# Kernel tuning notes

Measured on AMD Instinct MI355X. Metric: run time of the kernel, lower is better.

Reference implementation:

```python
import jax, jax.numpy as jnp
import numpy as np

B, T, D, H = 2, 2048, 768, 12
HD = D // H  # head_dim = 64


def setup_inputs() -> dict:
    key = jax.random.key(0)
    ks = jax.random.split(key, 5)
    s = 0.02
    return {
        "x": jax.random.normal(ks[0], (B, T, D), dtype=jnp.float32),
        "w_qkv": jax.random.normal(ks[1], (D, 3 * D), dtype=jnp.float32) * s,
        "b_qkv": jax.random.normal(ks[2], (3 * D,), dtype=jnp.float32) * s,
        "w_out": jax.random.normal(ks[3], (D, D), dtype=jnp.float32) * s,
        "b_out": jax.random.normal(ks[4], (D,), dtype=jnp.float32) * s,
    }


def reference(x, w_qkv, b_qkv, w_out, b_out):
    Bx, Tx, C = x.shape
    qkv = x @ w_qkv + b_qkv                       # [B,T,3C]
    q, k, v = jnp.split(qkv, 3, axis=-1)
    # [B,H,T,hd]
    q = q.reshape(Bx, Tx, H, HD).transpose(0, 2, 1, 3)
    k = k.reshape(Bx, Tx, H, HD).transpose(0, 2, 1, 3)
    v = v.reshape(Bx, Tx, H, HD).transpose(0, 2, 1, 3)
    scale = 1.0 / jnp.sqrt(jnp.float32(HD))
    attn = jnp.einsum('bhqd,bhkd->bhqk', q, k) * scale  # [B,H,T,T]
    causal = jnp.tril(jnp.ones((Tx, Tx), dtype=bool))
    attn = jnp.where(causal, attn, -jnp.inf)
    attn = jax.nn.softmax(attn, axis=-1)
    y = jnp.einsum('bhqk,bhkd->bhqd', attn, v)          # [B,H,T,hd]
    y = y.transpose(0, 2, 1, 3).reshape(Bx, Tx, C)
    return y @ w_out + b_out
```

## Files before the change

### kernel.cpp

```cpp
#include <hip/hip_runtime.h>
#include <math.h>

typedef __attribute__((ext_vector_type(8))) __bf16 bf16x8;
typedef __attribute__((ext_vector_type(4))) __bf16 bf16x4;
typedef __attribute__((ext_vector_type(4))) float f32x4;

#define GLOAD_LDS16(gsrc, ldst) \
  __builtin_amdgcn_global_load_lds((__attribute__((address_space(1))) const void*)(gsrc), \
                                   (__attribute__((address_space(3))) void*)(ldst), 16, 0, 0)

__device__ __forceinline__ float fexp2(float x) {
#if __has_builtin(__builtin_amdgcn_exp2f)
  return __builtin_amdgcn_exp2f(x);
#else
  return exp2f(x);
#endif
}

__global__ void cvt_bf16_kernel(const float* __restrict__ in, __bf16* __restrict__ out, int n4) {
  int i = blockIdx.x * 256 + threadIdx.x;
  if (i < n4) {
    float4 f = ((const float4*)in)[i];
    bf16x4 o;
    o[0] = (__bf16)f.x; o[1] = (__bf16)f.y; o[2] = (__bf16)f.z; o[3] = (__bf16)f.w;
    ((bf16x4*)out)[i] = o;
  }
}

__global__ __launch_bounds__(256)
void cvtT_bf16_kernel(const float* __restrict__ in, __bf16* __restrict__ out, int R, int C) {
  __shared__ float t[32][33];
  int c0 = blockIdx.x * 32, r0 = blockIdx.y * 32;
  int tc = threadIdx.x & 31, tr = threadIdx.x >> 5;
#pragma unroll
  for (int i = 0; i < 4; ++i)
    t[tr + 8 * i][tc] = in[(size_t)(r0 + tr + 8 * i) * C + c0 + tc];
  __syncthreads();
#pragma unroll
  for (int i = 0; i < 4; ++i)
    out[(size_t)(c0 + tr + 8 * i) * R + r0 + tc] = (__bf16)t[tc][tr + 8 * i];
}

template<int EPI, int BM, int BN, int WAVES, int WGM, int WGN, int BUFS>
__global__ __launch_bounds__(WAVES * 64, 3)
void gemm_tn_kernel(const __bf16* __restrict__ A, const __bf16* __restrict__ Bm,
                    const float* __restrict__ bias, float* __restrict__ outF,
                    __bf16* __restrict__ qo, __bf16* __restrict__ ko, __bf16* __restrict__ vo,
                    int M, int N, int K, int NBX, int NNX, int PPX) {
  constexpr int NTA = BM / 16, NTB = BN / 16;
  constexpr int NA = 2 * NTA;
  constexpr int NSEG = 2 * NTA + 2 * NTB;
  constexpr int LPTH = (NSEG + WAVES - 1) / WAVES;
  constexpr int LPTR = NSEG % WAVES;
  constexpr int LLO = (LPTR == 0) ? LPTH : LPTH - 1;
  constexpr int AM = NTA / WGM;
  constexpr int BNF = NTB / WGN;
  const int lane = threadIdx.x & 63;
  const int wave = threadIdx.x >> 6;
  const int r16 = lane & 15, g = lane >> 4;
  const int id = blockIdx.x;
  const int xcd = id & 7, slot = id >> 3;
  const int nxn = NBX / NNX;
  const int mg = xcd / nxn, ng = xcd % nxn;
  const int lp = slot / NNX, ln = slot - (slot / NNX) * NNX;
  const int mBase = (mg * PPX + lp) * BM, nBase = (ng * NNX + ln) * BN;
  __shared__ __align__(16) __bf16 lds[BUFS][NSEG * 512];

  f32x4 acc[AM][BNF];
#pragma unroll
  for (int i = 0; i < AM; ++i)
#pragma unroll
    for (int j = 0; j < BNF; ++j) acc[i][j] = (f32x4){0.f, 0.f, 0.f, 0.f};

  const int mw = (wave / WGN) * AM;
  const int nw = (wave % WGN) * BNF;

  auto stage = [&](int ke, int b) {
#pragma unroll
    for (int i = 0; i < LPTH; ++i) {
      int s = wave + i * WAVES;
      if (LPTR == 0 || s < NSEG) {
        int isB = (s >= NA);
        int sb = isB ? s - NA : s;
        int nt = isB ? NTB : NTA;
        int ks = sb / nt, t8 = sb - ks * nt;
        int row = (isB ? nBase : mBase) + t8 * 16 + r16;
        const __bf16* src = (isB ? Bm : A) + (size_t)row * K + ke + ks * 32 + g * 8;
        GLOAD_LDS16(src, &lds[b][s * 512]);
      }
    }
  };

  auto mfma_step = [&](const __bf16* L) {
#pragma unroll
    for (int ks = 0; ks < 2; ++ks) {
      bf16x8 af[AM], bfr[BNF];
#pragma unroll
      for (int i = 0; i < AM; ++i)
        af[i] = *(const bf16x8*)&L[((ks * NTA + mw + i) * 64 + lane) * 8];
#pragma unroll
      for (int j = 0; j < BNF; ++j)
        bfr[j] = *(const bf16x8*)&L[((NA + ks * NTB + nw + j) * 64 + lane) * 8];
      __builtin_amdgcn_s_setprio(1);
#pragma unroll
      for (int i = 0; i < AM; ++i)
#pragma unroll
        for (int j = 0; j < BNF; ++j)
          acc[i][j] = __builtin_amdgcn_mfma_f32_16x16x32_bf16(af[i], bfr[j], acc[i][j], 0, 0, 0);
      __builtin_amdgcn_s_setprio(0);
    }
  };

  const int nt = K >> 6;
  if constexpr (BUFS == 2) {
    stage(0, 0);
    int cur = 0;
    for (int t = 0; t < nt; ++t) {
      __syncthreads();
      if (t + 1 < nt) stage((t + 1) << 6, cur ^ 1);
      mfma_step(lds[cur]);
      cur ^= 1;
    }
  } else {
    stage(0, 0);
    stage(64, 1);
    int cur = 0;
    for (int t = 0; t < nt; ++t) {
      if (t + 1 < nt) {
        if (LPTR != 0 && wave < LPTR) asm volatile("s_waitcnt vmcnt(%0)" :: "i"(LPTH) : "memory");
        else                          asm volatile("s_waitcnt vmcnt(%0)" :: "i"(LLO) : "memory");
      } else {
        asm volatile("s_waitcnt vmcnt(0)" ::: "memory");
      }
      __builtin_amdgcn_sched_barrier(0);
      __builtin_amdgcn_s_barrier();
      __builtin_amdgcn_sched_barrier(0);
      int nxt = cur + 2; if (nxt >= 3) nxt -= 3;
      if (t + 2 < nt) stage((t + 2) << 6, nxt);
      mfma_step(lds[cur]);
      if (++cur == 3) cur = 0;
    }
  }

#pragma unroll
  for (int i = 0; i < AM; ++i) {
#pragma unroll
    for (int j = 0; j < BNF; ++j) {
      int c = nBase + (nw + j) * 16 + r16;
      float bb = bias[c];
#pragma unroll
      for (int e = 0; e < 4; ++e) {
        int r = mBase + (mw + i) * 16 + g * 4 + e;
        float val = acc[i][j][e] + bb;
        if (EPI == 0) {
          int which = c / 768;
          int cc = c - which * 768;
          int hh = cc >> 6, dd = cc & 63;
          int bI = r >> 11, tt = r & 2047;
          if (which == 0) {
            qo[(((size_t)(bI * 12 + hh)) * 2048 + tt) * 64 + dd] = (__bf16)(val * 0.180336880f);
          } else if (which == 1) {
            ko[(((size_t)(bI * 12 + hh)) * 2048 + tt) * 64 + dd] = (__bf16)val;
          } else {
            vo[(((size_t)(bI * 12 + hh)) * 64 + dd) * 2048 + tt] = (__bf16)val;
          }
        } else {
          outF[(size_t)r * N + c] = val;
        }
      }
    }
  }
}

__global__ __launch_bounds__(256, 3)
void attn_kernel(const __bf16* __restrict__ qg, const __bf16* __restrict__ kg,
                 const __bf16* __restrict__ vtg, __bf16* __restrict__ yatt) {
  const int id = blockIdx.x;
  const int chunk = id & 7, within = id >> 3;
  const int bh = chunk * 3 + (within >> 4);
  const int u = within & 15;
  const int lane = threadIdx.x & 63, wave = threadIdx.x >> 6;
  const int r16 = lane & 15, g = lane >> 4;
  const int bI = bh / 12, h = bh - bI * 12;
  const size_t headoff = (size_t)bh * 2048 * 64;
  const __bf16* Q = qg + headoff;
  const __bf16* Kh = kg + headoff;
  const __bf16* VT = vtg + headoff;

  __shared__ __align__(16) __bf16 Kbuf[2][4096];
  __shared__ __align__(16) __bf16 Vbuf[2][4096];
  __shared__ __align__(16) __bf16 Plds[4][16][72];

  const int myTile = (wave == 0) ? (63 - 2 * u) : (wave == 1) ? (62 - 2 * u)
                   : (wave == 2) ? (2 * u)      : (2 * u + 1);
  const int myKt = (myTile >> 1) + 1;
  const int Kmax = 32 - u;

  const int row0 = myTile * 32 + r16;
  const int row1 = myTile * 32 + 16 + r16;

  bf16x8 qf[2][2];
#pragma unroll
  for (int ks = 0; ks < 2; ++ks) {
    qf[0][ks] = *(const bf16x8*)&Q[(size_t)row0 * 64 + ks * 32 + g * 8];
    qf[1][ks] = *(const bf16x8*)&Q[(size_t)row1 * 64 + ks * 32 + g * 8];
  }

  int srow[2], scl[2];
#pragma unroll
  for (int i = 0; i < 2; ++i) {
    int c = (i * 4 + wave) * 64 + lane;
    srow[i] = c >> 3;
    scl[i] = (c & 7) ^ (srow[i] & 7);
  }
  auto stage = [&](int kt, int b) {
#pragma unroll
    for (int i = 0; i < 2; ++i) {
      GLOAD_LDS16(&Kh[(size_t)(kt * 64 + srow[i]) * 64 + scl[i] * 8], &Kbuf[b][(i * 4 + wave) * 512]);
      GLOAD_LDS16(&VT[(size_t)srow[i] * 2048 + kt * 64 + scl[i] * 8], &Vbuf[b][(i * 4 + wave) * 512]);
    }
  };

  f32x4 o0[4], o1[4];
#pragma unroll
  for (int j = 0; j < 4; ++j) { o0[j] = (f32x4){0.f,0.f,0.f,0.f}; o1[j] = (f32x4){0.f,0.f,0.f,0.f}; }
  float l0 = 0.f, l1 = 0.f;

  stage(0, 0);
  for (int kt = 0; kt < Kmax; ++kt) {
    const int cur = kt & 1;
    __syncthreads();
    if (kt + 1 < Kmax) stage(kt + 1, cur ^ 1);
    if (kt < myKt) {
      f32x4 st0[4], st1[4];
#pragma unroll
      for (int j = 0; j < 4; ++j) { st0[j] = (f32x4){0.f,0.f,0.f,0.f}; st1[j] = (f32x4){0.f,0.f,0.f,0.f}; }
      __builtin_amdgcn_s_setprio(1);
#pragma unroll
      for (int ks = 0; ks < 2; ++ks)
#pragma unroll
        for (int j = 0; j < 4; ++j) {
          int row = j * 16 + r16;
          int cp = (ks * 4 + g) ^ (row & 7);
          bf16x8 kf = *(const bf16x8*)&Kbuf[cur][(row * 8 + cp) * 8];
          st0[j] = __builtin_amdgcn_mfma_f32_16x16x32_bf16(kf, qf[0][ks], st0[j], 0, 0, 0);
          st1[j] = __builtin_amdgcn_mfma_f32_16x16x32_bf16(kf, qf[1][ks], st1[j], 0, 0, 0);
        }
      __builtin_amdgcn_s_setprio(0);
      bf16x8 vf[2][4];
#pragma unroll
      for (int ks = 0; ks < 2; ++ks)
#pragma unroll
        for (int dj = 0; dj < 4; ++dj) {
          int row = dj * 16 + r16;
          int cp = (ks * 4 + g) ^ (row & 7);
          vf[ks][dj] = *(const bf16x8*)&Vbuf[cur][(row * 8 + cp) * 8];
        }
      const bool lastT = (kt == myKt - 1);
      if (lastT) {
#pragma unroll
        for (int j = 0; j < 4; ++j)
#pragma unroll
          for (int e = 0; e < 4; ++e) {
            int k = kt * 64 + j * 16 + 4 * g + e;
            if (k > row0) st0[j][e] = -INFINITY;
            if (k > row1) st1[j][e] = -INFINITY;
          }
      }
      float ls0 = 0.f, ls1 = 0.f;
#pragma unroll
      for (int j = 0; j < 4; ++j)
#pragma unroll
        for (int e = 0; e < 4; ++e) {
          float p0 = fexp2(st0[j][e]);
          float p1 = fexp2(st1[j][e]);
          st0[j][e] = p0; ls0 += p0;
          st1[j][e] = p1; ls1 += p1;
        }
      ls0 += __shfl_xor(ls0, 16, 64); ls0 += __shfl_xor(ls0, 32, 64); l0 += ls0;
      ls1 += __shfl_xor(ls1, 16, 64); ls1 += __shfl_xor(ls1, 32, 64); l1 += ls1;
#pragma unroll
      for (int j = 0; j < 4; ++j) {
        bf16x4 pk;
#pragma unroll
        for (int e = 0; e < 4; ++e) pk[e] = (__bf16)st0[j][e];
        *(bf16x4*)&Plds[wave][r16][j * 16 + 4 * g] = pk;
      }
      __builtin_amdgcn_s_setprio(1);
#pragma unroll
      for (int ks = 0; ks < 2; ++ks) {
        bf16x8 pf = *(const bf16x8*)&Plds[wave][r16][ks * 32 + g * 8];
#pragma unroll
        for (int dj = 0; dj < 4; ++dj)
          o0[dj] = __builtin_amdgcn_mfma_f32_16x16x32_bf16(vf[ks][dj], pf, o0[dj], 0, 0, 0);
      }
      __builtin_amdgcn_s_setprio(0);
#pragma unroll
      for (int j = 0; j < 4; ++j) {
        bf16x4 pk;
#pragma unroll
        for (int e = 0; e < 4; ++e) pk[e] = (__bf16)st1[j][e];
        *(bf16x4*)&Plds[wave][r16][j * 16 + 4 * g] = pk;
      }
      __builtin_amdgcn_s_setprio(1);
#pragma unroll
      for (int ks = 0; ks < 2; ++ks) {
        bf16x8 pf = *(const bf16x8*)&Plds[wave][r16][ks * 32 + g * 8];
#pragma unroll
        for (int dj = 0; dj < 4; ++dj)
          o1[dj] = __builtin_amdgcn_mfma_f32_16x16x32_bf16(vf[ks][dj], pf, o1[dj], 0, 0, 0);
      }
      __builtin_amdgcn_s_setprio(0);
    }
  }

  float inv0 = 1.0f / l0, inv1 = 1.0f / l1;
#pragma unroll
  for (int dj = 0; dj < 4; ++dj) {
    bf16x4 ov0, ov1;
#pragma unroll
    for (int e = 0; e < 4; ++e) { ov0[e] = (__bf16)(o0[dj][e] * inv0); ov1[e] = (__bf16)(o1[dj][e] * inv1); }
    *(bf16x4*)&yatt[((size_t)(bI * 2048 + row0)) * 768 + h * 64 + dj * 16 + 4 * g] = ov0;
    *(bf16x4*)&yatt[((size_t)(bI * 2048 + row1)) * 768 + h * 64 + dj * 16 + 4 * g] = ov1;
  }
}

extern "C" void kernel_launch(void* const* d_in, const int* in_sizes, int n_in,
                              void* d_out, int out_size, void* d_ws, size_t ws_size,
                              hipStream_t stream) {
  (void)in_sizes; (void)n_in; (void)out_size; (void)ws_size;
  const float* x     = (const float*)d_in[0];
  const float* w_qkv = (const float*)d_in[1];
  const float* b_qkv = (const float*)d_in[2];
  const float* w_out = (const float*)d_in[3];
  const float* b_out = (const float*)d_in[4];
  float* out = (float*)d_out;

  char* ws = (char*)d_ws;
  __bf16* xb    = (__bf16*)(ws);
  __bf16* wqkvT = (__bf16*)(ws + 6291456);
  __bf16* woT   = (__bf16*)(ws + 9830400);
  __bf16* qb    = (__bf16*)(ws + 11010048);
  __bf16* kb    = (__bf16*)(ws + 17301504);
  __bf16* vtb   = (__bf16*)(ws + 23592960);
  __bf16* yatt  = (__bf16*)(ws + 29884416);

  cvt_bf16_kernel<<<3072, 256, 0, stream>>>(x, xb, 786432);
  cvtT_bf16_kernel<<<dim3(72, 24), 256, 0, stream>>>(w_qkv, wqkvT, 768, 2304);
  cvtT_bf16_kernel<<<dim3(24, 24), 256, 0, stream>>>(w_out, woT, 768, 768);
  gemm_tn_kernel<0, 128, 288, 12, 2, 6, 3><<<256, 768, 0, stream>>>(
      xb, wqkvT, b_qkv, nullptr, qb, kb, vtb, 4096, 2304, 768, 8, 1, 32);
  attn_kernel<<<384, 256, 0, stream>>>(qb, kb, vtb, yatt);
  gemm_tn_kernel<1, 64, 96, 4, 2, 2, 3><<<512, 256, 0, stream>>>(
      yatt, woT, b_out, out, nullptr, nullptr, nullptr, 4096, 768, 768, 8, 4, 16);
}
```

Before: 116.7 us.

## Balance causal attention work by pairing long and short row tiles per wave

Each wave now owns half of a long (late) query tile and half of its mirrored short (early) tile, instead of whole long or whole short tiles. Every wave therefore runs a similar number of K/V iterations, which removes idle waves during the tail of the block's loop. The block-to-head mapping also changes to interleave heads with u via division by 3, which alters the order in which blocks run. The cost is extra per-iteration branching on the short-tile condition and a different register layout.

```diff
diff --git a/kernel.cpp b/kernel.cpp
--- a/kernel.cpp
+++ b/kernel.cpp
@@ -177,8 +177,9 @@
                  const __bf16* __restrict__ vtg, __bf16* __restrict__ yatt) {
   const int id = blockIdx.x;
   const int chunk = id & 7, within = id >> 3;
-  const int bh = chunk * 3 + (within >> 4);
-  const int u = within & 15;
+  const int u = within / 3;
+  const int bh = chunk * 3 + (within - u * 3);
+  const int Kmax = 32 - u, Ka = u + 1;
   const int lane = threadIdx.x & 63, wave = threadIdx.x >> 6;
   const int r16 = lane & 15, g = lane >> 4;
   const int bI = bh / 12, h = bh - bI * 12;
@@ -191,19 +192,16 @@
   __shared__ __align__(16) __bf16 Vbuf[2][4096];
   __shared__ __align__(16) __bf16 Plds[4][16][72];
 
-  const int myTile = (wave == 0) ? (63 - 2 * u) : (wave == 1) ? (62 - 2 * u)
-                   : (wave == 2) ? (2 * u)      : (2 * u + 1);
-  const int myKt = (myTile >> 1) + 1;
-  const int Kmax = 32 - u;
-
-  const int row0 = myTile * 32 + r16;
-  const int row1 = myTile * 32 + 16 + r16;
-
-  bf16x8 qf[2][2];
+  const int ptile = 63 - 2 * u - (wave >> 1);
+  const int atile = 2 * u + (wave >> 1);
+  const int rowP = ptile * 32 + (wave & 1) * 16 + r16;
+  const int rowA = atile * 32 + (wave & 1) * 16 + r16;
+
+  bf16x8 qfp[2], qfa[2];
 #pragma unroll
   for (int ks = 0; ks < 2; ++ks) {
-    qf[0][ks] = *(const bf16x8*)&Q[(size_t)row0 * 64 + ks * 32 + g * 8];
-    qf[1][ks] = *(const bf16x8*)&Q[(size_t)row1 * 64 + ks * 32 + g * 8];
+    qfp[ks] = *(const bf16x8*)&Q[(size_t)rowP * 64 + ks * 32 + g * 8];
+    qfa[ks] = *(const bf16x8*)&Q[(size_t)rowA * 64 + ks * 32 + g * 8];
   }
 
   int srow[2], scl[2];
@@ -221,70 +219,92 @@
     }
   };
 
-  f32x4 o0[4], o1[4];
-#pragma unroll
-  for (int j = 0; j < 4; ++j) { o0[j] = (f32x4){0.f,0.f,0.f,0.f}; o1[j] = (f32x4){0.f,0.f,0.f,0.f}; }
-  float l0 = 0.f, l1 = 0.f;
+  f32x4 op[4], oa[4];
+#pragma unroll
+  for (int j = 0; j < 4; ++j) { op[j] = (f32x4){0.f,0.f,0.f,0.f}; oa[j] = (f32x4){0.f,0.f,0.f,0.f}; }
+  float lp = 0.f, la = 0.f;
 
   stage(0, 0);
   for (int kt = 0; kt < Kmax; ++kt) {
     const int cur = kt & 1;
     __syncthreads();
     if (kt + 1 < Kmax) stage(kt + 1, cur ^ 1);
-    if (kt < myKt) {
-      f32x4 st0[4], st1[4];
-#pragma unroll
-      for (int j = 0; j < 4; ++j) { st0[j] = (f32x4){0.f,0.f,0.f,0.f}; st1[j] = (f32x4){0.f,0.f,0.f,0.f}; }
-      __builtin_amdgcn_s_setprio(1);
-#pragma unroll
-      for (int ks = 0; ks < 2; ++ks)
-#pragma unroll
-        for (int j = 0; j < 4; ++j) {
-          int row = j * 16 + r16;
-          int cp = (ks * 4 + g) ^ (row & 7);
-          bf16x8 kf = *(const bf16x8*)&Kbuf[cur][(row * 8 + cp) * 8];
-          st0[j] = __builtin_amdgcn_mfma_f32_16x16x32_bf16(kf, qf[0][ks], st0[j], 0, 0, 0);
-          st1[j] = __builtin_amdgcn_mfma_f32_16x16x32_bf16(kf, qf[1][ks], st1[j], 0, 0, 0);
+    const bool dualA = (kt < Ka);
+    f32x4 stp[4], sta[4];
+#pragma unroll
+    for (int j = 0; j < 4; ++j) { stp[j] = (f32x4){0.f,0.f,0.f,0.f}; sta[j] = (f32x4){0.f,0.f,0.f,0.f}; }
+    __builtin_amdgcn_s_setprio(1);
+#pragma unroll
+    for (int ks = 0; ks < 2; ++ks)
+#pragma unroll
+      for (int j = 0; j < 4; ++j) {
+        int row = j * 16 + r16;
+        int cp = (ks * 4 + g) ^ (row & 7);
+        bf16x8 kf = *(const bf16x8*)&Kbuf[cur][(row * 8 + cp) * 8];
+        stp[j] = __builtin_amdgcn_mfma_f32_16x16x32_bf16(kf, qfp[ks], stp[j], 0, 0, 0);
+        if (dualA) sta[j] = __builtin_amdgcn_mfma_f32_16x16x32_bf16(kf, qfa[ks], sta[j], 0, 0, 0);
+      }
+    __builtin_amdgcn_s_setprio(0);
+    bf16x8 vf[2][4];
+#pragma unroll
+    for (int ks = 0; ks < 2; ++ks)
+#pragma unroll
+      for (int dj = 0; dj < 4; ++dj) {
+        int row = dj * 16 + r16;
+        int cp = (ks * 4 + g) ^ (row & 7);
+        vf[ks][dj] = *(const bf16x8*)&Vbuf[cur][(row * 8 + cp) * 8];
+      }
+    if (kt == Kmax - 1) {
+#pragma unroll
+      for (int j = 0; j < 4; ++j)
+#pragma unroll
+        for (int e = 0; e < 4; ++e)
+          if (kt * 64 + j * 16 + 4 * g + e > rowP) stp[j][e] = -INFINITY;
+    }
+    if (dualA && kt == Ka - 1) {
+#pragma unroll
+      for (int j = 0; j < 4; ++j)
+#pragma unroll
+        for (int e = 0; e < 4; ++e)
+          if (kt * 64 + j * 16 + 4 * g + e > rowA) sta[j][e] = -INFINITY;
+    }
+    float lsp = 0.f, lsa = 0.f;
+#pragma unroll
+    for (int j = 0; j < 4; ++j)
+#pragma unroll
+      for (int e = 0; e < 4; ++e) {
+        float pv = fexp2(stp[j][e]);
+        stp[j][e] = pv; lsp += pv;
+        if (dualA) {
+          float av = fexp2(sta[j][e]);
+          sta[j][e] = av; lsa += av;
         }
-      __builtin_amdgcn_s_setprio(0);
-      bf16x8 vf[2][4];
-#pragma unroll
-      for (int ks = 0; ks < 2; ++ks)
-#pragma unroll
-        for (int dj = 0; dj < 4; ++dj) {
-          int row = dj * 16 + r16;
-          int cp = (ks * 4 + g) ^ (row & 7);
-          vf[ks][dj] = *(const bf16x8*)&Vbuf[cur][(row * 8 + cp) * 8];
-        }
-      const bool lastT = (kt == myKt - 1);
-      if (lastT) {
-#pragma unroll
-        for (int j = 0; j < 4; ++j)
-#pragma unroll
-          for (int e = 0; e < 4; ++e) {
-            int k = kt * 64 + j * 16 + 4 * g + e;
-            if (k > row0) st0[j][e] = -INFINITY;
-            if (k > row1) st1[j][e] = -INFINITY;
-          }
-      }
-      float ls0 = 0.f, ls1 = 0.f;
-#pragma unroll
-      for (int j = 0; j < 4; ++j)
-#pragma unroll
-        for (int e = 0; e < 4; ++e) {
-          float p0 = fexp2(st0[j][e]);
-          float p1 = fexp2(st1[j][e]);
-          st0[j][e] = p0; ls0 += p0;
-          st1[j][e] = p1; ls1 += p1;
-        }
-      ls0 += __shfl_xor(ls0, 16, 64); ls0 += __shfl_xor(ls0, 32, 64); l0 += ls0;
-      ls1 += __shfl_xor(ls1, 16, 64); ls1 += __shfl_xor(ls1, 32, 64); l1 += ls1;
+      }
+    lsp += __shfl_xor(lsp, 16, 64); lsp += __shfl_xor(lsp, 32, 64); lp += lsp;
+    if (dualA) { lsa += __shfl_xor(lsa, 16, 64); lsa += __shfl_xor(lsa, 32, 64); la += lsa; }
+#pragma unroll
+    for (int j = 0; j < 4; ++j) {
+      bf16x4 pk;
+#pragma unroll
+      for (int e = 0; e < 4; ++e) pk[e] = (__bf16)stp[j][e];
+      *(bf16x4*)&Plds[wave][r16][j * 16 + 4 * g] = pk;
+    }
+    __builtin_amdgcn_s_setprio(1);
+#pragma unroll
+    for (int ks = 0; ks < 2; ++ks) {
+      bf16x8 pf = *(const bf16x8*)&Plds[wave][r16][ks * 32 + g * 8];
+#pragma unroll
+      for (int dj = 0; dj < 4; ++dj)
+        op[dj] = __builtin_amdgcn_mfma_f32_16x16x32_bf16(vf[ks][dj], pf, op[dj], 0, 0, 0);
+    }
+    __builtin_amdgcn_s_setprio(0);
+    if (dualA) {
 #pragma unroll
       for (int j = 0; j < 4; ++j) {
-        bf16x4 pk;
-#pragma unroll
-        for (int e = 0; e < 4; ++e) pk[e] = (__bf16)st0[j][e];
-        *(bf16x4*)&Plds[wave][r16][j * 16 + 4 * g] = pk;
+        bf16x4 ak;
+#pragma unroll
+        for (int e = 0; e < 4; ++e) ak[e] = (__bf16)sta[j][e];
+        *(bf16x4*)&Plds[wave][r16][j * 16 + 4 * g] = ak;
       }
       __builtin_amdgcn_s_setprio(1);
 #pragma unroll
@@ -292,36 +312,20 @@
         bf16x8 pf = *(const bf16x8*)&Plds[wave][r16][ks * 32 + g * 8];
 #pragma unroll
         for (int dj = 0; dj < 4; ++dj)
-          o0[dj] = __builtin_amdgcn_mfma_f32_16x16x32_bf16(vf[ks][dj], pf, o0[dj], 0, 0, 0);
+          oa[dj] = __builtin_amdgcn_mfma_f32_16x16x32_bf16(vf[ks][dj], pf, oa[dj], 0, 0, 0);
       }
       __builtin_amdgcn_s_setprio(0);
-#pragma unroll
-      for (int j = 0; j < 4; ++j) {
-        bf16x4 pk;
-#pragma unroll
-        for (int e = 0; e < 4; ++e) pk[e] = (__bf16)st1[j][e];
-        *(bf16x4*)&Plds[wave][r16][j * 16 + 4 * g] = pk;
-      }
-      __builtin_amdgcn_s_setprio(1);
-#pragma unroll
-      for (int ks = 0; ks < 2; ++ks) {
-        bf16x8 pf = *(const bf16x8*)&Plds[wave][r16][ks * 32 + g * 8];
-#pragma unroll
-        for (int dj = 0; dj < 4; ++dj)
-          o1[dj] = __builtin_amdgcn_mfma_f32_16x16x32_bf16(vf[ks][dj], pf, o1[dj], 0, 0, 0);
-      }
-      __builtin_amdgcn_s_setprio(0);
-    }
-  }
-
-  float inv0 = 1.0f / l0, inv1 = 1.0f / l1;
+    }
+  }
+
+  float invp = 1.0f / lp, inva = 1.0f / la;
 #pragma unroll
   for (int dj = 0; dj < 4; ++dj) {
-    bf16x4 ov0, ov1;
-#pragma unroll
-    for (int e = 0; e < 4; ++e) { ov0[e] = (__bf16)(o0[dj][e] * inv0); ov1[e] = (__bf16)(o1[dj][e] * inv1); }
-    *(bf16x4*)&yatt[((size_t)(bI * 2048 + row0)) * 768 + h * 64 + dj * 16 + 4 * g] = ov0;
-    *(bf16x4*)&yatt[((size_t)(bI * 2048 + row1)) * 768 + h * 64 + dj * 16 + 4 * g] = ov1;
+    bf16x4 ovp, ova;
+#pragma unroll
+    for (int e = 0; e < 4; ++e) { ovp[e] = (__bf16)(op[dj][e] * invp); ova[e] = (__bf16)(oa[dj][e] * inva); }
+    *(bf16x4*)&yatt[((size_t)(bI * 2048 + rowP)) * 768 + h * 64 + dj * 16 + 4 * g] = ovp;
+    *(bf16x4*)&yatt[((size_t)(bI * 2048 + rowA)) * 768 + h * 64 + dj * 16 + 4 * g] = ova;
   }
 }
 
```

Measured after the change: 116.5 us. Within noise of the previous version (-0.1%).
